# Performance work log

Measured on AMD Instinct MI355X. Metric: run time of the kernel, lower is better.

## Reference

```python
import jax, jax.numpy as jnp
import numpy as np

H, D, BD = 4, 128, 128   # num_heads, head_dim, bias_dim
QDIM = KDIM = 64
VDIM = 1
N = 512
EPS = 1e-5

def mish(x):
    return x * jnp.tanh(jax.nn.softplus(x))

def layernorm(x, g, b):
    m = jnp.mean(x, axis=-1, keepdims=True)
    v = jnp.var(x, axis=-1, keepdims=True)
    return (x - m) * jax.lax.rsqrt(v + EPS) * g + b

def _xavier(k, shape):
    fan_out, fan_in = shape
    lim = np.sqrt(6.0 / (fan_in + fan_out)).astype(np.float32)
    return jax.random.uniform(k, shape, jnp.float32, -lim, lim)

def setup_inputs() -> dict:
    key = jax.random.key(0)
    ks = jax.random.split(key, 12)
    return {
        "q": jax.random.normal(ks[0], (N, QDIM), jnp.float32),
        "k": jax.random.normal(ks[1], (N, KDIM), jnp.float32),
        "v": jax.random.normal(ks[2], (N, VDIM), jnp.float32),
        "bias": jax.random.uniform(ks[3], (N, N, BD), jnp.float32),
        "Wq": _xavier(ks[4], (H * D, QDIM)), "bq": jnp.zeros((H * D,), jnp.float32),
        "Wk": _xavier(ks[5], (H * D, KDIM)), "bk": jnp.zeros((H * D,), jnp.float32),
        "Wqo": _xavier(ks[6], (QDIM, H * D)), "bqo": jnp.zeros((QDIM,), jnp.float32),
        "Wko": _xavier(ks[7], (KDIM, H * D)), "bko": jnp.zeros((KDIM,), jnp.float32),
        "q_ln_g": jnp.ones((QDIM,), jnp.float32), "q_ln_b": jnp.zeros((QDIM,), jnp.float32),
        "k_ln_g": jnp.ones((KDIM,), jnp.float32), "k_ln_b": jnp.zeros((KDIM,), jnp.float32),
        "Wb": _xavier(ks[8], (H * BD, BD)), "bb_": jnp.zeros((H * BD,), jnp.float32),
        "Wbo": _xavier(ks[9], (BD, H * BD)), "bbo": jnp.zeros((BD,), jnp.float32),
    }

def reference(q, k, v, bias, Wq, bq, Wk, bk, Wqo, bqo, Wko, bko,
              q_ln_g, q_ln_b, k_ln_g, k_ln_b, Wb, bb_, Wbo, bbo):
    Nq, Nk = q.shape[0], k.shape[0]
    # q/k projections -> [N, H, D]
    pq = (q @ Wq.T + bq).reshape(Nq, H, D)
    pk = (k @ Wk.T + bk).reshape(Nk, H, D)
    # distance bias: Linear(BD -> H*BD), per-head L2 norm -> [H, Nq, Nk]
    bias_p = bias @ Wb.T + bb_                                  # [Nq, Nk, H*BD]
    diffs = jnp.linalg.norm(bias_p.reshape(Nq, Nk, H, BD), axis=-1)  # [Nq, Nk, H]
    diffs = jnp.transpose(diffs, (2, 0, 1))                     # [H, Nq, Nk]
    # scaled dot product attention with additive distance bias
    logits = jnp.einsum('qhd,khd->hqk', pq, pk) / np.sqrt(D).astype(np.float32) + diffs
    attn = jax.nn.softmax(logits, axis=-1)                      # [H, Nq, Nk]
    vals = jnp.einsum('hqk,kv->hqv', attn, v)                   # v shared across heads
    # values.permute(1,0,2).reshape(Nq, vdim*H) then mean over last dim
    vals_mean = jnp.mean(jnp.transpose(vals, (1, 0, 2)).reshape(Nq, H * VDIM),
                         axis=-1, keepdims=True)                # [Nq, 1]
    # torch does proj.permute(1,2,0).reshape(N, H*D): (d, h)-major flattening
    pq_flat = jnp.transpose(pq, (0, 2, 1)).reshape(Nq, D * H)
    pk_flat = jnp.transpose(pk, (0, 2, 1)).reshape(Nk, D * H)
    q_new = layernorm(q + mish(pq_flat @ Wqo.T + bqo), q_ln_g, q_ln_b)
    k_new = layernorm(k + mish(pk_flat @ Wko.T + bko), k_ln_g, k_ln_b)
    bias_out = mish(bias_p @ Wbo.T + bbo)                       # [Nq, Nk, BD]
    return (q_new, k_new, vals_mean, bias_out)
```

## Files before the change

kernel.cpp:

```cpp
#include <hip/hip_runtime.h>

#define NN 512
#define MROWS (NN*NN)
#define LDK 136

typedef __attribute__((ext_vector_type(8))) short short8;
typedef __attribute__((ext_vector_type(4))) float floatx4;

__device__ __forceinline__ unsigned short f2bf(float f) {
    union { float f; unsigned u; } x; x.f = f;
    unsigned r = x.u + 0x7fffu + ((x.u >> 16) & 1u);
    return (unsigned short)(r >> 16);
}

__global__ void prep_kernel(const float* __restrict__ Wb, const float* __restrict__ Wbo,
                            unsigned short* __restrict__ wbf) {
    int i = blockIdx.x * 256 + threadIdx.x;
    float v = (i < 65536) ? Wb[i] : Wbo[i - 65536];
    wbf[i] = f2bf(v);
}

__global__ __launch_bounds__(256) void proj_kernel(
    const float* __restrict__ q, const float* __restrict__ k,
    const float* __restrict__ Wq, const float* __restrict__ bq,
    const float* __restrict__ Wk, const float* __restrict__ bk,
    float* __restrict__ pq, float* __restrict__ pk)
{
    __shared__ float xs[64];
    int b = blockIdx.x;
    int n = b & 511;
    int is_k = b >> 9;
    const float* x  = is_k ? k  : q;
    const float* W  = is_k ? Wk : Wq;
    const float* bi = is_k ? bk : bq;
    float* out      = is_k ? pk : pq;
    int tid = threadIdx.x;
    if (tid < 16)
        reinterpret_cast<float4*>(xs)[tid] = reinterpret_cast<const float4*>(x + n*64)[tid];
    __syncthreads();
    #pragma unroll
    for (int jj = 0; jj < 2; ++jj) {
        int j = jj*256 + tid;
        const float4* wr = reinterpret_cast<const float4*>(W + j*64);
        float acc = bi[j];
        #pragma unroll
        for (int c = 0; c < 16; ++c) {
            float4 w4 = wr[c];
            float4 x4 = reinterpret_cast<const float4*>(xs)[c];
            acc += x4.x*w4.x + x4.y*w4.y + x4.z*w4.z + x4.w*w4.w;
        }
        out[n*512 + j] = acc;
    }
}

__global__ __launch_bounds__(256, 2) void bias_kernel(
    const float* __restrict__ bias, const unsigned short* __restrict__ wb_bf,
    const float* __restrict__ bb, const unsigned short* __restrict__ wbo_bf,
    const float* __restrict__ bbo, float* __restrict__ bias_out,
    float* __restrict__ diffs)
{
    __shared__ unsigned short lA[64*LDK];
    __shared__ unsigned short lW[128*LDK];
    __shared__ unsigned short lP[64*LDK];
    __shared__ float sq[64];

    const int tid  = threadIdx.x;
    const int wave = tid >> 6, lane = tid & 63;
    const int quad = lane >> 4, l16 = lane & 15;
    const long row0 = (long)blockIdx.x * 64;
    const int colb = wave * 32;

    {
        const float* src = bias + row0 * 128;
        #pragma unroll
        for (int i = 0; i < 8; ++i) {
            int flat = i*1024 + tid*4;
            int r = flat >> 7, c = flat & 127;
            float4 v = *reinterpret_cast<const float4*>(src + flat);
            ushort4 o = { f2bf(v.x), f2bf(v.y), f2bf(v.z), f2bf(v.w) };
            *reinterpret_cast<ushort4*>(&lA[r*LDK + c]) = o;
        }
    }

    floatx4 acc2[4][2];
    #pragma unroll
    for (int mt = 0; mt < 4; ++mt)
        #pragma unroll
        for (int nt = 0; nt < 2; ++nt) acc2[mt][nt] = (floatx4){0.f,0.f,0.f,0.f};

    for (int h = 0; h < 4; ++h) {
        #pragma unroll
        for (int i = 0; i < 8; ++i) {
            int flat = i*2048 + tid*8;
            int r = flat >> 7, c = flat & 127;
            *reinterpret_cast<uint4*>(&lW[r*LDK + c]) =
                *reinterpret_cast<const uint4*>(wb_bf + h*16384 + flat);
        }
        if (tid < 64) sq[tid] = 0.f;
        __syncthreads();

        floatx4 acc1[4][2];
        #pragma unroll
        for (int mt = 0; mt < 4; ++mt)
            #pragma unroll
            for (int nt = 0; nt < 2; ++nt) acc1[mt][nt] = (floatx4){0.f,0.f,0.f,0.f};
        #pragma unroll
        for (int kk = 0; kk < 4; ++kk) {
            short8 a[4], bfr[2];
            #pragma unroll
            for (int mt = 0; mt < 4; ++mt)
                a[mt] = *reinterpret_cast<const short8*>(&lA[(mt*16 + l16)*LDK + kk*32 + quad*8]);
            #pragma unroll
            for (int nt = 0; nt < 2; ++nt)
                bfr[nt] = *reinterpret_cast<const short8*>(&lW[(colb + nt*16 + l16)*LDK + kk*32 + quad*8]);
            #pragma unroll
            for (int mt = 0; mt < 4; ++mt)
                #pragma unroll
                for (int nt = 0; nt < 2; ++nt)
                    acc1[mt][nt] = __builtin_amdgcn_mfma_f32_16x16x32_bf16(a[mt], bfr[nt], acc1[mt][nt], 0, 0, 0);
        }

        float bbv0 = bb[h*128 + colb + l16];
        float bbv1 = bb[h*128 + colb + 16 + l16];
        #pragma unroll
        for (int mt = 0; mt < 4; ++mt) {
            #pragma unroll
            for (int r = 0; r < 4; ++r) {
                float c0 = acc1[mt][0][r] + bbv0;
                float c1 = acc1[mt][1][r] + bbv1;
                float s = c0*c0 + c1*c1;
                s += __shfl_xor(s, 1);
                s += __shfl_xor(s, 2);
                s += __shfl_xor(s, 4);
                s += __shfl_xor(s, 8);
                int m = mt*16 + quad*4 + r;
                if (l16 == 0) atomicAdd(&sq[m], s);
                lP[m*LDK + colb + l16]      = f2bf(c0);
                lP[m*LDK + colb + 16 + l16] = f2bf(c1);
            }
        }
        __syncthreads();
        if (tid < 64) diffs[(long)h*MROWS + row0 + tid] = sqrtf(sq[tid]);

        #pragma unroll
        for (int i = 0; i < 8; ++i) {
            int flat = i*2048 + tid*8;
            int r = flat >> 7, c = flat & 127;
            *reinterpret_cast<uint4*>(&lW[r*LDK + c]) =
                *reinterpret_cast<const uint4*>(wbo_bf + r*512 + h*128 + c);
        }
        __syncthreads();

        #pragma unroll
        for (int kk = 0; kk < 4; ++kk) {
            short8 a[4], bfr[2];
            #pragma unroll
            for (int mt = 0; mt < 4; ++mt)
                a[mt] = *reinterpret_cast<const short8*>(&lP[(mt*16 + l16)*LDK + kk*32 + quad*8]);
            #pragma unroll
            for (int nt = 0; nt < 2; ++nt)
                bfr[nt] = *reinterpret_cast<const short8*>(&lW[(colb + nt*16 + l16)*LDK + kk*32 + quad*8]);
            #pragma unroll
            for (int mt = 0; mt < 4; ++mt)
                #pragma unroll
                for (int nt = 0; nt < 2; ++nt)
                    acc2[mt][nt] = __builtin_amdgcn_mfma_f32_16x16x32_bf16(a[mt], bfr[nt], acc2[mt][nt], 0, 0, 0);
        }
        __syncthreads();
    }

    #pragma unroll
    for (int nt = 0; nt < 2; ++nt) {
        int n2 = colb + nt*16 + l16;
        float bv = bbo[n2];
        #pragma unroll
        for (int mt = 0; mt < 4; ++mt) {
            #pragma unroll
            for (int r = 0; r < 4; ++r) {
                int m = mt*16 + quad*4 + r;
                float s = acc2[mt][nt][r] + bv;
                float e = __expf(s);
                float u = 1.f + e, u2 = u*u;
                float msh = (s > 15.f) ? s : s * (u2 - 1.f) / (u2 + 1.f);
                bias_out[(row0 + m)*128 + n2] = msh;
            }
        }
    }
}

__global__ __launch_bounds__(256) void qk_kernel(
    const float* __restrict__ pq, const float* __restrict__ pk,
    float* __restrict__ logits)
{
    __shared__ float A[64*128];
    __shared__ float BT[128*64];
    int blk = blockIdx.x;
    int kt = blk & 7, h = (blk >> 3) & 3, qt = blk >> 5;
    int tid = threadIdx.x;

    #pragma unroll
    for (int i = 0; i < 8; ++i) {
        int flat = i*1024 + tid*4;
        int r = flat >> 7, c = flat & 127;
        *reinterpret_cast<float4*>(&A[flat]) =
            *reinterpret_cast<const float4*>(pq + (size_t)(qt*64 + r)*512 + h*128 + c);
    }
    {
        int kk = tid & 63, g = tid >> 6;
        #pragma unroll
        for (int i = 0; i < 8; ++i) {
            int d0 = g*32 + i*4;
            float4 vv = *reinterpret_cast<const float4*>(pk + (size_t)(kt*64 + kk)*512 + h*128 + d0);
            BT[(d0+0)*64 + kk] = vv.x;
            BT[(d0+1)*64 + kk] = vv.y;
            BT[(d0+2)*64 + kk] = vv.z;
            BT[(d0+3)*64 + kk] = vv.w;
        }
    }
    __syncthreads();

    int qg = tid >> 4, kg = tid & 15;
    int qs = qg*4, ks = kg*4;
    float acc[4][4] = {};
    for (int d = 0; d < 128; d += 4) {
        float a_[4][4], b_[4][4];
        #pragma unroll
        for (int i = 0; i < 4; ++i) {
            float4 av = *reinterpret_cast<const float4*>(&A[(qs+i)*128 + d]);
            a_[i][0] = av.x; a_[i][1] = av.y; a_[i][2] = av.z; a_[i][3] = av.w;
        }
        #pragma unroll
        for (int dd = 0; dd < 4; ++dd) {
            float4 bv = *reinterpret_cast<const float4*>(&BT[(d+dd)*64 + ks]);
            b_[dd][0] = bv.x; b_[dd][1] = bv.y; b_[dd][2] = bv.z; b_[dd][3] = bv.w;
        }
        #pragma unroll
        for (int i = 0; i < 4; ++i)
            #pragma unroll
            for (int j = 0; j < 4; ++j)
                acc[i][j] += a_[i][0]*b_[0][j] + a_[i][1]*b_[1][j]
                           + a_[i][2]*b_[2][j] + a_[i][3]*b_[3][j];
    }

    const float scale = 0.088388347648318447f;
    #pragma unroll
    for (int i = 0; i < 4; ++i) {
        size_t off = (size_t)h*MROWS + (size_t)(qt*64 + qs + i)*512 + kt*64 + ks;
        float4* p = reinterpret_cast<float4*>(logits + off);
        float4 dv = *p;
        dv.x = fmaf(acc[i][0], scale, dv.x);
        dv.y = fmaf(acc[i][1], scale, dv.y);
        dv.z = fmaf(acc[i][2], scale, dv.z);
        dv.w = fmaf(acc[i][3], scale, dv.w);
        *p = dv;
    }
}

__global__ __launch_bounds__(256) void attnval_kernel(
    const float* __restrict__ logits, const float* __restrict__ v,
    float* __restrict__ vmean)
{
    __shared__ float red[32];
    int qrow = blockIdx.x, tid = threadIdx.x;
    int wid = tid >> 6;
    float vsum = 0.f;
    float v0 = v[tid], v1 = v[tid + 256];
    for (int h = 0; h < 4; ++h) {
        const float* lr = logits + (size_t)h*MROWS + (size_t)qrow*512;
        float l0 = lr[tid], l1 = lr[tid + 256];
        float m = fmaxf(l0, l1);
        #pragma unroll
        for (int o = 1; o < 64; o <<= 1) m = fmaxf(m, __shfl_xor(m, o));
        if ((tid & 63) == 0) red[wid] = m;
        __syncthreads();
        m = fmaxf(fmaxf(red[0], red[1]), fmaxf(red[2], red[3]));
        float e0 = __expf(l0 - m), e1 = __expf(l1 - m);
        float s = e0 + e1;
        float sv = e0*v0 + e1*v1;
        #pragma unroll
        for (int o = 1; o < 64; o <<= 1) { s += __shfl_xor(s, o); sv += __shfl_xor(sv, o); }
        __syncthreads();
        if ((tid & 63) == 0) { red[8 + wid] = s; red[16 + wid] = sv; }
        __syncthreads();
        float S  = red[8]  + red[9]  + red[10] + red[11];
        float SV = red[16] + red[17] + red[18] + red[19];
        vsum += SV / S;
        __syncthreads();
    }
    if (tid == 0) vmean[qrow] = vsum * 0.25f;
}

__global__ __launch_bounds__(256) void qkout_kernel(
    const float* __restrict__ p, const float* __restrict__ x,
    const float* __restrict__ W, const float* __restrict__ bo,
    const float* __restrict__ g, const float* __restrict__ be,
    float* __restrict__ out)
{
    __shared__ float pr[512];
    __shared__ float red[256];
    int n = blockIdx.x, tid = threadIdx.x;
    if (tid < 128)
        reinterpret_cast<float4*>(pr)[tid] = reinterpret_cast<const float4*>(p + (size_t)n*512)[tid];
    __syncthreads();
    int o = tid >> 2, part = tid & 3;
    const float4* wr = reinterpret_cast<const float4*>(W + o*512 + part*128);
    float acc = 0.f;
    #pragma unroll
    for (int c = 0; c < 32; ++c) {
        float4 w4 = wr[c];
        int base = part*32 + c;
        acc += pr[base]*w4.x + pr[128 + base]*w4.y + pr[256 + base]*w4.z + pr[384 + base]*w4.w;
    }
    red[tid] = acc;
    __syncthreads();
    if (tid < 64) {
        float s = red[tid*4] + red[tid*4+1] + red[tid*4+2] + red[tid*4+3] + bo[tid];
        float e = __expf(s);
        float u = 1.f + e, u2 = u*u;
        float msh = (s > 15.f) ? s : s * (u2 - 1.f) / (u2 + 1.f);
        float val = x[n*64 + tid] + msh;
        float m = val, m2 = val*val;
        #pragma unroll
        for (int off = 1; off < 64; off <<= 1) { m += __shfl_xor(m, off); m2 += __shfl_xor(m2, off); }
        m *= (1.f/64.f); m2 *= (1.f/64.f);
        float var = m2 - m*m;
        out[n*64 + tid] = (val - m) * rsqrtf(var + 1e-5f) * g[tid] + be[tid];
    }
}

extern "C" void kernel_launch(void* const* d_in, const int* in_sizes, int n_in,
                              void* d_out, int out_size, void* d_ws, size_t ws_size,
                              hipStream_t stream) {
    const float* q    = (const float*)d_in[0];
    const float* k    = (const float*)d_in[1];
    const float* v    = (const float*)d_in[2];
    const float* bias = (const float*)d_in[3];
    const float* Wq   = (const float*)d_in[4];
    const float* bq   = (const float*)d_in[5];
    const float* Wk   = (const float*)d_in[6];
    const float* bk   = (const float*)d_in[7];
    const float* Wqo  = (const float*)d_in[8];
    const float* bqo  = (const float*)d_in[9];
    const float* Wko  = (const float*)d_in[10];
    const float* bko  = (const float*)d_in[11];
    const float* qlg  = (const float*)d_in[12];
    const float* qlb  = (const float*)d_in[13];
    const float* klg  = (const float*)d_in[14];
    const float* klb  = (const float*)d_in[15];
    const float* Wb   = (const float*)d_in[16];
    const float* bb   = (const float*)d_in[17];
    const float* Wbo  = (const float*)d_in[18];
    const float* bbo  = (const float*)d_in[19];

    float* out = (float*)d_out;
    float* ws  = (float*)d_ws;
    float* diffs = ws;
    float* pq    = ws + 4*MROWS;
    float* pk    = pq + MROWS;
    unsigned short* wbf = (unsigned short*)(pk + MROWS);

    float* q_new = out;
    float* k_new = out + 32768;
    float* vmean = out + 65536;
    float* b_out = out + 66048;

    prep_kernel<<<dim3(512), dim3(256), 0, stream>>>(Wb, Wbo, wbf);
    proj_kernel<<<dim3(1024), dim3(256), 0, stream>>>(q, k, Wq, bq, Wk, bk, pq, pk);
    bias_kernel<<<dim3(4096), dim3(256), 0, stream>>>(bias, wbf, bb, wbf + 65536, bbo, b_out, diffs);
    qk_kernel<<<dim3(256), dim3(256), 0, stream>>>(pq, pk, diffs);
    attnval_kernel<<<dim3(512), dim3(256), 0, stream>>>(diffs, v, vmean);
    qkout_kernel<<<dim3(512), dim3(256), 0, stream>>>(pq, q, Wqo, bqo, qlg, qlb, q_new);
    qkout_kernel<<<dim3(512), dim3(256), 0, stream>>>(pk, k, Wko, bko, klg, klb, k_new);
}
```

Measured before the change: 479.8 us.

## Restructure bias kernel: 32x32 MFMA with weights from global, smaller LDS, coalesced stores

The bias kernel now uses 32x32x16 bf16 MFMA with the weight as the A operand, read directly from global memory (L2-resident) rather than staged through LDS. This removes the lW buffer and its per-head syncs, shrinks shared memory so four blocks can share a CU, and lets the per-head norm reduction need only one shuffle. Output goes through an LDS transpose so the final stores are coalesced float4 writes. The prep and projection kernels are merged into one launch. The risk is higher global-load latency for the weight fragments and heavier register pressure under the tighter launch bound.

```diff
diff --git a/kernel.cpp b/kernel.cpp
--- a/kernel.cpp
+++ b/kernel.cpp
@@ -5,7 +5,7 @@
 #define LDK 136
 
 typedef __attribute__((ext_vector_type(8))) short short8;
-typedef __attribute__((ext_vector_type(4))) float floatx4;
+typedef __attribute__((ext_vector_type(16))) float floatx16;
 
 __device__ __forceinline__ unsigned short f2bf(float f) {
     union { float f; unsigned u; } x; x.f = f;
@@ -13,28 +13,36 @@
     return (unsigned short)(r >> 16);
 }
 
-__global__ void prep_kernel(const float* __restrict__ Wb, const float* __restrict__ Wbo,
-                            unsigned short* __restrict__ wbf) {
-    int i = blockIdx.x * 256 + threadIdx.x;
-    float v = (i < 65536) ? Wb[i] : Wbo[i - 65536];
-    wbf[i] = f2bf(v);
-}
-
-__global__ __launch_bounds__(256) void proj_kernel(
+__device__ __forceinline__ floatx16 zero16() {
+    floatx16 z;
+    #pragma unroll
+    for (int i = 0; i < 16; ++i) z[i] = 0.f;
+    return z;
+}
+
+__global__ __launch_bounds__(256) void pre_kernel(
     const float* __restrict__ q, const float* __restrict__ k,
     const float* __restrict__ Wq, const float* __restrict__ bq,
     const float* __restrict__ Wk, const float* __restrict__ bk,
-    float* __restrict__ pq, float* __restrict__ pk)
-{
+    float* __restrict__ pq, float* __restrict__ pk,
+    const float* __restrict__ Wb, const float* __restrict__ Wbo,
+    unsigned short* __restrict__ wbf)
+{
+    int b = blockIdx.x;
+    int tid = threadIdx.x;
+    if (b >= 1024) {
+        int i = (b - 1024) * 256 + tid;
+        float v = (i < 65536) ? Wb[i] : Wbo[i - 65536];
+        wbf[i] = f2bf(v);
+        return;
+    }
     __shared__ float xs[64];
-    int b = blockIdx.x;
     int n = b & 511;
     int is_k = b >> 9;
     const float* x  = is_k ? k  : q;
     const float* W  = is_k ? Wk : Wq;
     const float* bi = is_k ? bk : bq;
     float* out      = is_k ? pk : pq;
-    int tid = threadIdx.x;
     if (tid < 16)
         reinterpret_cast<float4*>(xs)[tid] = reinterpret_cast<const float4*>(x + n*64)[tid];
     __syncthreads();
@@ -53,138 +61,154 @@
     }
 }
 
-__global__ __launch_bounds__(256, 2) void bias_kernel(
+__global__ __launch_bounds__(256, 4) void bias_kernel(
     const float* __restrict__ bias, const unsigned short* __restrict__ wb_bf,
     const float* __restrict__ bb, const unsigned short* __restrict__ wbo_bf,
     const float* __restrict__ bbo, float* __restrict__ bias_out,
     float* __restrict__ diffs)
 {
-    __shared__ unsigned short lA[64*LDK];
-    __shared__ unsigned short lW[128*LDK];
-    __shared__ unsigned short lP[64*LDK];
-    __shared__ float sq[64];
-
-    const int tid  = threadIdx.x;
-    const int wave = tid >> 6, lane = tid & 63;
-    const int quad = lane >> 4, l16 = lane & 15;
+    __shared__ __align__(16) char smem[34816 + 256];
+    unsigned short* lA = (unsigned short*)smem;
+    unsigned short* lP = (unsigned short*)(smem + 17408);
+    float* sq = (float*)(smem + 34816);
+    float* lT = (float*)smem;
+
+    const int tid = threadIdx.x;
+    const int w   = tid >> 6;
+    const int l   = tid & 63;
+    const int l31 = l & 31;
+    const int qh  = l >> 5;
     const long row0 = (long)blockIdx.x * 64;
-    const int colb = wave * 32;
 
     {
         const float* src = bias + row0 * 128;
         #pragma unroll
-        for (int i = 0; i < 8; ++i) {
-            int flat = i*1024 + tid*4;
-            int r = flat >> 7, c = flat & 127;
-            float4 v = *reinterpret_cast<const float4*>(src + flat);
-            ushort4 o = { f2bf(v.x), f2bf(v.y), f2bf(v.z), f2bf(v.w) };
-            *reinterpret_cast<ushort4*>(&lA[r*LDK + c]) = o;
-        }
-    }
-
-    floatx4 acc2[4][2];
-    #pragma unroll
-    for (int mt = 0; mt < 4; ++mt)
-        #pragma unroll
-        for (int nt = 0; nt < 2; ++nt) acc2[mt][nt] = (floatx4){0.f,0.f,0.f,0.f};
-
-    for (int h = 0; h < 4; ++h) {
-        #pragma unroll
-        for (int i = 0; i < 8; ++i) {
+        for (int i = 0; i < 4; ++i) {
             int flat = i*2048 + tid*8;
             int r = flat >> 7, c = flat & 127;
-            *reinterpret_cast<uint4*>(&lW[r*LDK + c]) =
-                *reinterpret_cast<const uint4*>(wb_bf + h*16384 + flat);
+            float4 v0 = *reinterpret_cast<const float4*>(src + flat);
+            float4 v1 = *reinterpret_cast<const float4*>(src + flat + 4);
+            ushort4 o0 = { f2bf(v0.x), f2bf(v0.y), f2bf(v0.z), f2bf(v0.w) };
+            ushort4 o1 = { f2bf(v1.x), f2bf(v1.y), f2bf(v1.z), f2bf(v1.w) };
+            *reinterpret_cast<ushort4*>(&lA[r*LDK + c])     = o0;
+            *reinterpret_cast<ushort4*>(&lA[r*LDK + c + 4]) = o1;
         }
         if (tid < 64) sq[tid] = 0.f;
-        __syncthreads();
-
-        floatx4 acc1[4][2];
-        #pragma unroll
-        for (int mt = 0; mt < 4; ++mt)
-            #pragma unroll
-            for (int nt = 0; nt < 2; ++nt) acc1[mt][nt] = (floatx4){0.f,0.f,0.f,0.f};
-        #pragma unroll
-        for (int kk = 0; kk < 4; ++kk) {
-            short8 a[4], bfr[2];
-            #pragma unroll
-            for (int mt = 0; mt < 4; ++mt)
-                a[mt] = *reinterpret_cast<const short8*>(&lA[(mt*16 + l16)*LDK + kk*32 + quad*8]);
-            #pragma unroll
-            for (int nt = 0; nt < 2; ++nt)
-                bfr[nt] = *reinterpret_cast<const short8*>(&lW[(colb + nt*16 + l16)*LDK + kk*32 + quad*8]);
-            #pragma unroll
-            for (int mt = 0; mt < 4; ++mt)
-                #pragma unroll
-                for (int nt = 0; nt < 2; ++nt)
-                    acc1[mt][nt] = __builtin_amdgcn_mfma_f32_16x16x32_bf16(a[mt], bfr[nt], acc1[mt][nt], 0, 0, 0);
-        }
-
-        float bbv0 = bb[h*128 + colb + l16];
-        float bbv1 = bb[h*128 + colb + 16 + l16];
-        #pragma unroll
-        for (int mt = 0; mt < 4; ++mt) {
+    }
+
+    floatx16 acc2[2];
+    acc2[0] = zero16(); acc2[1] = zero16();
+
+    const unsigned short* wbbase  = wb_bf  + (w*32 + l31)*128 + qh*8;
+    const unsigned short* wbobase = wbo_bf + (w*32 + l31)*512 + qh*8;
+
+    __syncthreads();
+
+    for (int h = 0; h < 4; ++h) {
+        floatx16 acc1[2];
+        acc1[0] = zero16(); acc1[1] = zero16();
+        const unsigned short* wa = wbbase + h*16384;
+        #pragma unroll
+        for (int kk = 0; kk < 8; ++kk) {
+            short8 afr = *reinterpret_cast<const short8*>(wa + kk*16);
+            short8 b0  = *reinterpret_cast<const short8*>(&lA[(l31)*LDK      + kk*16 + qh*8]);
+            short8 b1  = *reinterpret_cast<const short8*>(&lA[(32 + l31)*LDK + kk*16 + qh*8]);
+            acc1[0] = __builtin_amdgcn_mfma_f32_32x32x16_bf16(afr, b0, acc1[0], 0, 0, 0);
+            acc1[1] = __builtin_amdgcn_mfma_f32_32x32x16_bf16(afr, b1, acc1[1], 0, 0, 0);
+        }
+
+        float4 bbq[4];
+        #pragma unroll
+        for (int s = 0; s < 4; ++s)
+            bbq[s] = *reinterpret_cast<const float4*>(bb + h*128 + w*32 + qh*4 + s*8);
+
+        float ssum[2];
+        ushort4 pk4[2][4];
+        #pragma unroll
+        for (int nt = 0; nt < 2; ++nt) {
+            float sa = 0.f;
+            #pragma unroll
+            for (int s = 0; s < 4; ++s) {
+                const float* bbp = (const float*)&bbq[s];
+                float v0 = acc1[nt][s*4+0] + bbp[0];
+                float v1 = acc1[nt][s*4+1] + bbp[1];
+                float v2 = acc1[nt][s*4+2] + bbp[2];
+                float v3 = acc1[nt][s*4+3] + bbp[3];
+                sa += v0*v0 + v1*v1 + v2*v2 + v3*v3;
+                pk4[nt][s] = (ushort4){ f2bf(v0), f2bf(v1), f2bf(v2), f2bf(v3) };
+            }
+            sa += __shfl_xor(sa, 32);
+            ssum[nt] = sa;
+        }
+
+        __syncthreads();
+
+        #pragma unroll
+        for (int nt = 0; nt < 2; ++nt) {
+            int m = nt*32 + l31;
+            #pragma unroll
+            for (int s = 0; s < 4; ++s)
+                *reinterpret_cast<ushort4*>(&lP[m*LDK + w*32 + qh*4 + s*8]) = pk4[nt][s];
+            if (l < 32) atomicAdd(&sq[m], ssum[nt]);
+        }
+
+        __syncthreads();
+
+        if (tid < 64) {
+            float s2 = sq[tid];
+            diffs[(long)h*MROWS + row0 + tid] = sqrtf(s2);
+            sq[tid] = 0.f;
+        }
+
+        const unsigned short* wo = wbobase + h*128;
+        #pragma unroll
+        for (int kk = 0; kk < 8; ++kk) {
+            short8 afr = *reinterpret_cast<const short8*>(wo + kk*16);
+            short8 b0  = *reinterpret_cast<const short8*>(&lP[(l31)*LDK      + kk*16 + qh*8]);
+            short8 b1  = *reinterpret_cast<const short8*>(&lP[(32 + l31)*LDK + kk*16 + qh*8]);
+            acc2[0] = __builtin_amdgcn_mfma_f32_32x32x16_bf16(afr, b0, acc2[0], 0, 0, 0);
+            acc2[1] = __builtin_amdgcn_mfma_f32_32x32x16_bf16(afr, b1, acc2[1], 0, 0, 0);
+        }
+    }
+
+    float4 bboq[4];
+    #pragma unroll
+    for (int s = 0; s < 4; ++s)
+        bboq[s] = *reinterpret_cast<const float4*>(bbo + w*32 + qh*4 + s*8);
+
+    float outs[2][16];
+    #pragma unroll
+    for (int nt = 0; nt < 2; ++nt) {
+        #pragma unroll
+        for (int s = 0; s < 4; ++s) {
+            const float* bp = (const float*)&bboq[s];
             #pragma unroll
             for (int r = 0; r < 4; ++r) {
-                float c0 = acc1[mt][0][r] + bbv0;
-                float c1 = acc1[mt][1][r] + bbv1;
-                float s = c0*c0 + c1*c1;
-                s += __shfl_xor(s, 1);
-                s += __shfl_xor(s, 2);
-                s += __shfl_xor(s, 4);
-                s += __shfl_xor(s, 8);
-                int m = mt*16 + quad*4 + r;
-                if (l16 == 0) atomicAdd(&sq[m], s);
-                lP[m*LDK + colb + l16]      = f2bf(c0);
-                lP[m*LDK + colb + 16 + l16] = f2bf(c1);
+                float x = acc2[nt][s*4+r] + bp[r];
+                float e = __expf(x);
+                float u = 1.f + e, u2 = u*u;
+                outs[nt][s*4+r] = (x > 15.f) ? x : x * (u2 - 1.f) / (u2 + 1.f);
             }
         }
-        __syncthreads();
-        if (tid < 64) diffs[(long)h*MROWS + row0 + tid] = sqrtf(sq[tid]);
-
-        #pragma unroll
-        for (int i = 0; i < 8; ++i) {
-            int flat = i*2048 + tid*8;
-            int r = flat >> 7, c = flat & 127;
-            *reinterpret_cast<uint4*>(&lW[r*LDK + c]) =
-                *reinterpret_cast<const uint4*>(wbo_bf + r*512 + h*128 + c);
-        }
-        __syncthreads();
-
-        #pragma unroll
-        for (int kk = 0; kk < 4; ++kk) {
-            short8 a[4], bfr[2];
-            #pragma unroll
-            for (int mt = 0; mt < 4; ++mt)
-                a[mt] = *reinterpret_cast<const short8*>(&lP[(mt*16 + l16)*LDK + kk*32 + quad*8]);
-            #pragma unroll
-            for (int nt = 0; nt < 2; ++nt)
-                bfr[nt] = *reinterpret_cast<const short8*>(&lW[(colb + nt*16 + l16)*LDK + kk*32 + quad*8]);
-            #pragma unroll
-            for (int mt = 0; mt < 4; ++mt)
-                #pragma unroll
-                for (int nt = 0; nt < 2; ++nt)
-                    acc2[mt][nt] = __builtin_amdgcn_mfma_f32_16x16x32_bf16(a[mt], bfr[nt], acc2[mt][nt], 0, 0, 0);
-        }
-        __syncthreads();
-    }
-
+    }
+
+    __syncthreads();
     #pragma unroll
     for (int nt = 0; nt < 2; ++nt) {
-        int n2 = colb + nt*16 + l16;
-        float bv = bbo[n2];
-        #pragma unroll
-        for (int mt = 0; mt < 4; ++mt) {
-            #pragma unroll
-            for (int r = 0; r < 4; ++r) {
-                int m = mt*16 + quad*4 + r;
-                float s = acc2[mt][nt][r] + bv;
-                float e = __expf(s);
-                float u = 1.f + e, u2 = u*u;
-                float msh = (s > 15.f) ? s : s * (u2 - 1.f) / (u2 + 1.f);
-                bias_out[(row0 + m)*128 + n2] = msh;
-            }
-        }
+        int m = nt*32 + l31;
+        #pragma unroll
+        for (int s = 0; s < 4; ++s)
+            #pragma unroll
+            for (int r = 0; r < 4; ++r)
+                lT[m*LDK + w*32 + qh*4 + s*8 + r] = outs[nt][s*4+r];
+    }
+    __syncthreads();
+    #pragma unroll
+    for (int i = 0; i < 8; ++i) {
+        int flat = i*1024 + tid*4;
+        int r = flat >> 7, c = flat & 127;
+        *reinterpret_cast<float4*>(bias_out + (row0 + r)*128 + c) =
+            *reinterpret_cast<const float4*>(&lT[r*LDK + c]);
     }
 }
 
@@ -364,8 +388,7 @@
     float* vmean = out + 65536;
     float* b_out = out + 66048;
 
-    prep_kernel<<<dim3(512), dim3(256), 0, stream>>>(Wb, Wbo, wbf);
-    proj_kernel<<<dim3(1024), dim3(256), 0, stream>>>(q, k, Wq, bq, Wk, bk, pq, pk);
+    pre_kernel<<<dim3(1536), dim3(256), 0, stream>>>(q, k, Wq, bq, Wk, bk, pq, pk, Wb, Wbo, wbf);
     bias_kernel<<<dim3(4096), dim3(256), 0, stream>>>(bias, wbf, bb, wbf + 65536, bbo, b_out, diffs);
     qk_kernel<<<dim3(256), dim3(256), 0, stream>>>(pq, pk, diffs);
     attnval_kernel<<<dim3(512), dim3(256), 0, stream>>>(diffs, v, vmean);
```

Result: faster. 447.4 us (-6.8%).
